# Performance work log

Hardware: AMD Instinct MI355X
Metric: run time of the kernel (lower is better)

Reference implementation:

```python
import jax, jax.numpy as jnp
import numpy as np

B, S, E, A, DK, H = 8, 2048, 256, 16, 64, 64  # batch, seq, embed, action, d_key, mlp hidden


def setup_inputs() -> dict:
    key = jax.random.key(0)
    ks = jax.random.split(key, 8)
    obs = jax.random.normal(ks[0], (B, S, E), dtype=jnp.float32)
    act = jnp.zeros((B, S, A), dtype=jnp.float32)  # one-hot actions; unused by forward
    # projection weights stored as [in, out] (torch Linear applies x @ W.T)
    Wq = jax.random.normal(ks[1], (E, DK), dtype=jnp.float32) / np.sqrt(E)
    Wk = jax.random.normal(ks[2], (E, DK), dtype=jnp.float32) / np.sqrt(E)
    Wv = jax.random.normal(ks[3], (E, DK), dtype=jnp.float32) / np.sqrt(E)
    W1 = jax.random.normal(ks[4], (DK, H), dtype=jnp.float32) / np.sqrt(DK)
    b1 = jnp.zeros((H,), dtype=jnp.float32)
    W2 = jax.random.normal(ks[5], (H, 1), dtype=jnp.float32) / np.sqrt(H)
    b2 = jnp.zeros((1,), dtype=jnp.float32)
    return dict(obs=obs, act=act, Wq=Wq, Wk=Wk, Wv=Wv, W1=W1, b1=b1, W2=W2, b2=b2)


def reference(obs, act, Wq, Wk, Wv, W1, b1, W2, b2):
    b, s, _ = obs.shape
    dk = Wq.shape[1]
    scale = dk ** -0.25  # applied to both q and k, net 1/sqrt(dk)
    q = (obs @ Wq) * scale          # [b, s, dk]
    k = (obs @ Wk) * scale          # [b, s, dk]
    v = obs @ Wv                    # [b, s, dk]
    scores = jnp.einsum('bqd,bkd->bqk', q, k)  # [b, s, s]
    causal = jnp.tril(jnp.ones((s, s), dtype=bool))
    scores = jnp.where(causal[None], scores, -jnp.inf)
    attn = jax.nn.softmax(scores, axis=2)      # [b, s, s]
    attn_out = jnp.einsum('bqk,bkd->bqd', attn, v)  # [b, s, dk]
    h = jax.nn.relu(attn_out.reshape(b * s, dk) @ W1 + b1)
    x = h @ W2 + b2                 # [b*s, 1]
    return (x, attn)
```

## Files before the change

### kernel.cpp

```cpp
#include <hip/hip_runtime.h>
#include <hip/hip_bf16.h>
#include <math.h>

#define NB 8
#define SQ 2048
#define NSP 8

typedef __attribute__((ext_vector_type(8))) short short8;
typedef __attribute__((ext_vector_type(4))) float f32x4;

__device__ __forceinline__ short f2bf(float f) {
    union { float f; unsigned u; } v; v.f = f;
    unsigned r = v.u + 0x7FFF + ((v.u >> 16) & 1);
    return (short)(r >> 16);
}

__global__ __launch_bounds__(256) void k_wt(const float* __restrict__ Wq,
                                            const float* __restrict__ Wk,
                                            const float* __restrict__ Wv,
                                            short* __restrict__ wt) {
    int o = blockIdx.x * 256 + threadIdx.x;
    int row = o >> 8, e = o & 255;
    int w = row >> 6, d = row & 63;
    const float* W = (w == 0) ? Wq : ((w == 1) ? Wk : Wv);
    wt[o] = f2bf(W[e * 64 + d]);
}

__global__ __launch_bounds__(256, 4) void k_proj(const float* __restrict__ obs,
                                                 const short* __restrict__ wt,
                                                 short* __restrict__ qw,
                                                 short* __restrict__ kw,
                                                 short* __restrict__ vt) {
    int tid = threadIdx.x, w = tid >> 6, l = tid & 63, lg = l >> 4, lc = l & 15;
    int r0 = blockIdx.x * 16;
    int arow = r0 + lc;
    f32x4 accq = {0.f,0.f,0.f,0.f}, acck = {0.f,0.f,0.f,0.f}, accv = {0.f,0.f,0.f,0.f};
    const short* wq = wt + (size_t)(w * 16 + lc) * 256;
    const short* wk = wt + (size_t)(64 + w * 16 + lc) * 256;
    const short* wv = wt + (size_t)(128 + w * 16 + lc) * 256;
    #pragma unroll
    for (int ks = 0; ks < 8; ++ks) {
        int e0 = ks * 32 + lg * 8;
        const float* ap = obs + (size_t)arow * 256 + e0;
        float4 f0 = *(const float4*)ap;
        float4 f1 = *(const float4*)(ap + 4);
        short8 a;
        a[0] = f2bf(f0.x); a[1] = f2bf(f0.y); a[2] = f2bf(f0.z); a[3] = f2bf(f0.w);
        a[4] = f2bf(f1.x); a[5] = f2bf(f1.y); a[6] = f2bf(f1.z); a[7] = f2bf(f1.w);
        accq = __builtin_amdgcn_mfma_f32_16x16x32_bf16(a, *(const short8*)(wq + e0), accq, 0, 0, 0);
        acck = __builtin_amdgcn_mfma_f32_16x16x32_bf16(a, *(const short8*)(wk + e0), acck, 0, 0, 0);
        accv = __builtin_amdgcn_mfma_f32_16x16x32_bf16(a, *(const short8*)(wv + e0), accv, 0, 0, 0);
    }
    const float scale = 0.35355339059327373f;
    __shared__ short ldsv[64][18];
    #pragma unroll
    for (int r = 0; r < 4; ++r) {
        int row = r0 + lg * 4 + r;
        qw[(size_t)row * 64 + w * 16 + lc] = f2bf(accq[r] * scale);
        kw[(size_t)row * 64 + w * 16 + lc] = f2bf(acck[r] * scale);
        ldsv[w * 16 + lc][lg * 4 + r] = f2bf(accv[r]);
    }
    __syncthreads();
    int b = r0 >> 11, s0 = r0 & 2047;
    int d = tid >> 2, sc = (tid & 3) * 4;
    short* dst = vt + (size_t)b * 64 * SQ + (size_t)d * SQ + s0 + sc;
    dst[0] = ldsv[d][sc]; dst[1] = ldsv[d][sc + 1];
    dst[2] = ldsv[d][sc + 2]; dst[3] = ldsv[d][sc + 3];
}

__global__ __launch_bounds__(256) void k_flash(const short* __restrict__ qw,
                                               const short* __restrict__ kw,
                                               const short* __restrict__ vt,
                                               float* __restrict__ op,
                                               float* __restrict__ lpart) {
    int qb = blockIdx.x, sp = blockIdx.y, b = blockIdx.z;
    if (sp > qb) return;
    int q0 = qb * 64;
    int tid = threadIdx.x, w = tid >> 6, l = tid & 63, lg = l >> 4, lc = l & 15;
    int r0 = q0 + w * 16;
    int eo = lg * 8;
    __shared__ short ldsP[4][16][72];
    const short* qbase = qw + (size_t)b * SQ * 64;
    const short* kbase = kw + (size_t)b * SQ * 64;
    const short* vbase = vt + (size_t)b * 64 * SQ;
    short8 qf0 = *(const short8*)(qbase + (size_t)(r0 + lc) * 64 + eo);
    short8 qf1 = *(const short8*)(qbase + (size_t)(r0 + lc) * 64 + 32 + eo);
    float lsum[4];
    f32x4 o[4];
    #pragma unroll
    for (int r = 0; r < 4; ++r) lsum[r] = 0.f;
    #pragma unroll
    for (int nj = 0; nj < 4; ++nj) o[nj] = (f32x4){0.f, 0.f, 0.f, 0.f};

    for (int kb = sp; kb <= qb; kb += NSP) {
        int k0 = kb * 64;
        f32x4 s[4];
        #pragma unroll
        for (int nj = 0; nj < 4; ++nj) s[nj] = (f32x4){0.f, 0.f, 0.f, 0.f};
        #pragma unroll
        for (int nj = 0; nj < 4; ++nj) {
            short8 kf = *(const short8*)(kbase + (size_t)(k0 + nj * 16 + lc) * 64 + eo);
            s[nj] = __builtin_amdgcn_mfma_f32_16x16x32_bf16(qf0, kf, s[nj], 0, 0, 0);
        }
        #pragma unroll
        for (int nj = 0; nj < 4; ++nj) {
            short8 kf = *(const short8*)(kbase + (size_t)(k0 + nj * 16 + lc) * 64 + 32 + eo);
            s[nj] = __builtin_amdgcn_mfma_f32_16x16x32_bf16(qf1, kf, s[nj], 0, 0, 0);
        }
        if (kb == qb) {
            #pragma unroll
            for (int nj = 0; nj < 4; ++nj)
                #pragma unroll
                for (int r = 0; r < 4; ++r)
                    if (k0 + nj * 16 + lc > r0 + lg * 4 + r) s[nj][r] = -INFINITY;
        }
        #pragma unroll
        for (int r = 0; r < 4; ++r) {
            float ps = 0.f;
            #pragma unroll
            for (int nj = 0; nj < 4; ++nj) {
                float p = __expf(s[nj][r]);
                ps += p;
                ldsP[w][lg * 4 + r][nj * 16 + lc] = f2bf(p);
            }
            ps += __shfl_xor(ps, 1);
            ps += __shfl_xor(ps, 2);
            ps += __shfl_xor(ps, 4);
            ps += __shfl_xor(ps, 8);
            lsum[r] += ps;
        }
        #pragma unroll
        for (int ks = 0; ks < 2; ++ks) {
            short8 pa = *(const short8*)&ldsP[w][lc][ks * 32 + lg * 8];
            #pragma unroll
            for (int nj = 0; nj < 4; ++nj) {
                short8 vf = *(const short8*)(vbase + (size_t)(nj * 16 + lc) * SQ + k0 + ks * 32 + eo);
                o[nj] = __builtin_amdgcn_mfma_f32_16x16x32_bf16(pa, vf, o[nj], 0, 0, 0);
            }
        }
    }
    size_t pb = ((size_t)sp * NB + b) * SQ;
    #pragma unroll
    for (int r = 0; r < 4; ++r) {
        int row = r0 + lg * 4 + r;
        if (lc == 0) lpart[pb + row] = lsum[r];
        #pragma unroll
        for (int nj = 0; nj < 4; ++nj)
            op[(pb + row) * 64 + nj * 16 + lc] = o[nj][r];
    }
}

__global__ __launch_bounds__(256) void k_combine(const float* __restrict__ op,
                                                 const float* __restrict__ lpart,
                                                 const float* __restrict__ W1,
                                                 const float* __restrict__ b1,
                                                 const float* __restrict__ W2,
                                                 const float* __restrict__ b2,
                                                 float* __restrict__ x,
                                                 float* __restrict__ linv) {
    int row0 = blockIdx.x * 8;
    int tid = threadIdx.x, w = tid >> 6, l = tid & 63;
    __shared__ float w1l[64][64];
    __shared__ float aol[8][64];
    {
        const float4* src = (const float4*)W1;
        float4* dst = (float4*)&w1l[0][0];
        #pragma unroll
        for (int i = 0; i < 4; ++i) dst[tid + i * 256] = src[tid + i * 256];
    }
    float inv2[2];
    #pragma unroll
    for (int rr = 0; rr < 2; ++rr) {
        int grow = row0 + w * 2 + rr;
        int b = grow >> 11, s = grow & 2047;
        int nsp = (s >> 6) + 1; if (nsp > NSP) nsp = NSP;
        float od = 0.f, lt = 0.f;
        for (int sp = 0; sp < nsp; ++sp) {
            size_t base = (size_t)(sp * NB + b) * SQ + s;
            od += op[base * 64 + l];
            lt += lpart[base];
        }
        float inv = 1.f / lt;
        inv2[rr] = inv;
        aol[w * 2 + rr][l] = od * inv;
        if (l == 0) linv[grow] = inv;
    }
    __syncthreads();
    #pragma unroll
    for (int rr = 0; rr < 2; ++rr) {
        int grow = row0 + w * 2 + rr;
        float t = b1[l];
        #pragma unroll 16
        for (int d = 0; d < 64; ++d) t += aol[w * 2 + rr][d] * w1l[d][l];
        float h = fmaxf(t, 0.f);
        float px = h * W2[l];
        px += __shfl_xor(px, 1);
        px += __shfl_xor(px, 2);
        px += __shfl_xor(px, 4);
        px += __shfl_xor(px, 8);
        px += __shfl_xor(px, 16);
        px += __shfl_xor(px, 32);
        if (l == 0) x[grow] = px + b2[0];
    }
    (void)inv2;
}

__global__ __launch_bounds__(256) void k_attnw(const short* __restrict__ qw,
                                               const short* __restrict__ kw,
                                               const float* __restrict__ linv,
                                               float* __restrict__ attn) {
    int kb = blockIdx.x, qb = blockIdx.y, b = blockIdx.z;
    int q0 = qb * 64, k0 = kb * 64;
    float* abase = attn + (size_t)b * SQ * SQ;
    int tid = threadIdx.x;
    if (kb > qb) {
        int row = q0 + (tid >> 2);
        float4* dst = (float4*)(abase + (size_t)row * SQ + k0 + (tid & 3) * 16);
        float4 z = {0.f, 0.f, 0.f, 0.f};
        dst[0] = z; dst[1] = z; dst[2] = z; dst[3] = z;
        return;
    }
    int w = tid >> 6, l = tid & 63, lg = l >> 4, lc = l & 15;
    int r0 = q0 + w * 16, eo = lg * 8;
    const short* qbase = qw + (size_t)b * SQ * 64;
    const short* kbase = kw + (size_t)b * SQ * 64;
    short8 qf0 = *(const short8*)(qbase + (size_t)(r0 + lc) * 64 + eo);
    short8 qf1 = *(const short8*)(qbase + (size_t)(r0 + lc) * 64 + 32 + eo);
    f32x4 s[4];
    #pragma unroll
    for (int nj = 0; nj < 4; ++nj) s[nj] = (f32x4){0.f, 0.f, 0.f, 0.f};
    #pragma unroll
    for (int nj = 0; nj < 4; ++nj) {
        short8 kf = *(const short8*)(kbase + (size_t)(k0 + nj * 16 + lc) * 64 + eo);
        s[nj] = __builtin_amdgcn_mfma_f32_16x16x32_bf16(qf0, kf, s[nj], 0, 0, 0);
    }
    #pragma unroll
    for (int nj = 0; nj < 4; ++nj) {
        short8 kf = *(const short8*)(kbase + (size_t)(k0 + nj * 16 + lc) * 64 + 32 + eo);
        s[nj] = __builtin_amdgcn_mfma_f32_16x16x32_bf16(qf1, kf, s[nj], 0, 0, 0);
    }
    #pragma unroll
    for (int r = 0; r < 4; ++r) {
        int row = r0 + lg * 4 + r;
        float iv = linv[(size_t)b * SQ + row];
        #pragma unroll
        for (int nj = 0; nj < 4; ++nj) {
            int col = k0 + nj * 16 + lc;
            float p = (col <= row) ? __expf(s[nj][r]) * iv : 0.f;
            abase[(size_t)row * SQ + col] = p;
        }
    }
}

extern "C" void kernel_launch(void* const* d_in, const int* in_sizes, int n_in,
                              void* d_out, int out_size, void* d_ws, size_t ws_size,
                              hipStream_t stream) {
    const float* obs = (const float*)d_in[0];
    const float* Wq  = (const float*)d_in[2];
    const float* Wk  = (const float*)d_in[3];
    const float* Wv  = (const float*)d_in[4];
    const float* W1  = (const float*)d_in[5];
    const float* b1  = (const float*)d_in[6];
    const float* W2  = (const float*)d_in[7];
    const float* b2  = (const float*)d_in[8];

    float* x    = (float*)d_out;
    float* attn = (float*)d_out + NB * SQ;

    float* op = attn;

    char* ws = (char*)d_ws;
    short* wt    = (short*)(ws);
    short* qw    = (short*)(ws + 131072);
    short* kw    = (short*)(ws + 2228224);
    short* vt    = (short*)(ws + 4325376);
    float* lpart = (float*)(ws + 6422528);
    float* linv  = (float*)(ws + 6946816);

    k_wt<<<dim3(192), dim3(256), 0, stream>>>(Wq, Wk, Wv, wt);
    k_proj<<<dim3(1024), dim3(256), 0, stream>>>(obs, wt, qw, kw, vt);
    k_flash<<<dim3(32, NSP, NB), dim3(256), 0, stream>>>(qw, kw, vt, op, lpart);
    k_combine<<<dim3(2048), dim3(256), 0, stream>>>(op, lpart, W1, b1, W2, b2, x, linv);
    k_attnw<<<dim3(32, 32, NB), dim3(256), 0, stream>>>(qw, kw, linv, attn);
}
```

Measured before the change: 158.8 us.

## Write unnormalized probabilities from flash kernel and rescale attention in separate pass

The flash kernel now stores exp(scores) straight into the attention output while it accumulates. A separate scaling kernel then multiplies by the inverse row sums and zeroes the upper triangle, replacing the kernel that recomputed QK^T. Row-sum reduction moves to its own small kernel, the partial-output buffer moves into workspace, and the number of key splits is halved. This removes the second QK^T recomputation but adds a read-modify-write pass over the lower-triangular attention matrix.

Result: faster. 140.4 us (-11.6%).

```diff
diff --git a/kernel.cpp b/kernel.cpp
--- a/kernel.cpp
+++ b/kernel.cpp
@@ -4,7 +4,7 @@
 
 #define NB 8
 #define SQ 2048
-#define NSP 8
+#define NSP 4
 
 typedef __attribute__((ext_vector_type(8))) short short8;
 typedef __attribute__((ext_vector_type(4))) float f32x4;
@@ -72,7 +72,8 @@
                                                const short* __restrict__ kw,
                                                const short* __restrict__ vt,
                                                float* __restrict__ op,
-                                               float* __restrict__ lpart) {
+                                               float* __restrict__ lpart,
+                                               float* __restrict__ attn) {
     int qb = blockIdx.x, sp = blockIdx.y, b = blockIdx.z;
     if (sp > qb) return;
     int q0 = qb * 64;
@@ -83,6 +84,7 @@
     const short* qbase = qw + (size_t)b * SQ * 64;
     const short* kbase = kw + (size_t)b * SQ * 64;
     const short* vbase = vt + (size_t)b * 64 * SQ;
+    float* abase = attn + (size_t)b * SQ * SQ;
     short8 qf0 = *(const short8*)(qbase + (size_t)(r0 + lc) * 64 + eo);
     short8 qf1 = *(const short8*)(qbase + (size_t)(r0 + lc) * 64 + 32 + eo);
     float lsum[4];
@@ -116,12 +118,14 @@
         }
         #pragma unroll
         for (int r = 0; r < 4; ++r) {
+            int row = r0 + lg * 4 + r;
             float ps = 0.f;
             #pragma unroll
             for (int nj = 0; nj < 4; ++nj) {
                 float p = __expf(s[nj][r]);
                 ps += p;
                 ldsP[w][lg * 4 + r][nj * 16 + lc] = f2bf(p);
+                abase[(size_t)row * SQ + k0 + nj * 16 + lc] = p;
             }
             ps += __shfl_xor(ps, 1);
             ps += __shfl_xor(ps, 2);
@@ -150,14 +154,23 @@
     }
 }
 
+__global__ __launch_bounds__(256) void k_lred(const float* __restrict__ lpart,
+                                              float* __restrict__ linv) {
+    int g = blockIdx.x * 256 + threadIdx.x;
+    int s = g & 2047, b = g >> 11;
+    int nsp = (s >> 6) + 1; if (nsp > NSP) nsp = NSP;
+    float t = 0.f;
+    for (int sp = 0; sp < nsp; ++sp) t += lpart[((size_t)sp * NB + b) * SQ + s];
+    linv[g] = 1.f / t;
+}
+
 __global__ __launch_bounds__(256) void k_combine(const float* __restrict__ op,
-                                                 const float* __restrict__ lpart,
+                                                 const float* __restrict__ linv,
                                                  const float* __restrict__ W1,
                                                  const float* __restrict__ b1,
                                                  const float* __restrict__ W2,
                                                  const float* __restrict__ b2,
-                                                 float* __restrict__ x,
-                                                 float* __restrict__ linv) {
+                                                 float* __restrict__ x) {
     int row0 = blockIdx.x * 8;
     int tid = threadIdx.x, w = tid >> 6, l = tid & 63;
     __shared__ float w1l[64][64];
@@ -168,22 +181,15 @@
         #pragma unroll
         for (int i = 0; i < 4; ++i) dst[tid + i * 256] = src[tid + i * 256];
     }
-    float inv2[2];
     #pragma unroll
     for (int rr = 0; rr < 2; ++rr) {
         int grow = row0 + w * 2 + rr;
         int b = grow >> 11, s = grow & 2047;
         int nsp = (s >> 6) + 1; if (nsp > NSP) nsp = NSP;
-        float od = 0.f, lt = 0.f;
-        for (int sp = 0; sp < nsp; ++sp) {
-            size_t base = (size_t)(sp * NB + b) * SQ + s;
-            od += op[base * 64 + l];
-            lt += lpart[base];
-        }
-        float inv = 1.f / lt;
-        inv2[rr] = inv;
-        aol[w * 2 + rr][l] = od * inv;
-        if (l == 0) linv[grow] = inv;
+        float od = 0.f;
+        for (int sp = 0; sp < nsp; ++sp)
+            od += op[(((size_t)sp * NB + b) * SQ + s) * 64 + l];
+        aol[w * 2 + rr][l] = od * linv[grow];
     }
     __syncthreads();
     #pragma unroll
@@ -202,53 +208,36 @@
         px += __shfl_xor(px, 32);
         if (l == 0) x[grow] = px + b2[0];
     }
-    (void)inv2;
-}
-
-__global__ __launch_bounds__(256) void k_attnw(const short* __restrict__ qw,
-                                               const short* __restrict__ kw,
-                                               const float* __restrict__ linv,
+}
+
+__global__ __launch_bounds__(256) void k_scale(const float* __restrict__ linv,
                                                float* __restrict__ attn) {
-    int kb = blockIdx.x, qb = blockIdx.y, b = blockIdx.z;
-    int q0 = qb * 64, k0 = kb * 64;
+    int csp = blockIdx.x, qb = blockIdx.y, b = blockIdx.z;
+    int tid = threadIdx.x, w = tid >> 6, l = tid & 63;
     float* abase = attn + (size_t)b * SQ * SQ;
-    int tid = threadIdx.x;
-    if (kb > qb) {
-        int row = q0 + (tid >> 2);
-        float4* dst = (float4*)(abase + (size_t)row * SQ + k0 + (tid & 3) * 16);
+    int colb = csp * 256 + l * 4;
+    if (csp * 4 > qb) {
         float4 z = {0.f, 0.f, 0.f, 0.f};
-        dst[0] = z; dst[1] = z; dst[2] = z; dst[3] = z;
+        #pragma unroll
+        for (int r = 0; r < 16; ++r) {
+            int row = qb * 64 + w * 16 + r;
+            *(float4*)(abase + (size_t)row * SQ + colb) = z;
+        }
         return;
     }
-    int w = tid >> 6, l = tid & 63, lg = l >> 4, lc = l & 15;
-    int r0 = q0 + w * 16, eo = lg * 8;
-    const short* qbase = qw + (size_t)b * SQ * 64;
-    const short* kbase = kw + (size_t)b * SQ * 64;
-    short8 qf0 = *(const short8*)(qbase + (size_t)(r0 + lc) * 64 + eo);
-    short8 qf1 = *(const short8*)(qbase + (size_t)(r0 + lc) * 64 + 32 + eo);
-    f32x4 s[4];
-    #pragma unroll
-    for (int nj = 0; nj < 4; ++nj) s[nj] = (f32x4){0.f, 0.f, 0.f, 0.f};
-    #pragma unroll
-    for (int nj = 0; nj < 4; ++nj) {
-        short8 kf = *(const short8*)(kbase + (size_t)(k0 + nj * 16 + lc) * 64 + eo);
-        s[nj] = __builtin_amdgcn_mfma_f32_16x16x32_bf16(qf0, kf, s[nj], 0, 0, 0);
-    }
-    #pragma unroll
-    for (int nj = 0; nj < 4; ++nj) {
-        short8 kf = *(const short8*)(kbase + (size_t)(k0 + nj * 16 + lc) * 64 + 32 + eo);
-        s[nj] = __builtin_amdgcn_mfma_f32_16x16x32_bf16(qf1, kf, s[nj], 0, 0, 0);
-    }
-    #pragma unroll
-    for (int r = 0; r < 4; ++r) {
-        int row = r0 + lg * 4 + r;
-        float iv = linv[(size_t)b * SQ + row];
-        #pragma unroll
-        for (int nj = 0; nj < 4; ++nj) {
-            int col = k0 + nj * 16 + lc;
-            float p = (col <= row) ? __expf(s[nj][r]) * iv : 0.f;
-            abase[(size_t)row * SQ + col] = p;
-        }
+    #pragma unroll
+    for (int r = 0; r < 16; ++r) {
+        int row = qb * 64 + w * 16 + r;
+        float inv = linv[(size_t)b * SQ + row];
+        int lim = row | 63;
+        float* p = abase + (size_t)row * SQ + colb;
+        float4 v = *(const float4*)p;
+        float4 o;
+        o.x = (colb + 0 <= lim) ? v.x * inv : 0.f;
+        o.y = (colb + 1 <= lim) ? v.y * inv : 0.f;
+        o.z = (colb + 2 <= lim) ? v.z * inv : 0.f;
+        o.w = (colb + 3 <= lim) ? v.w * inv : 0.f;
+        *(float4*)p = o;
     }
 }
 
@@ -267,19 +256,19 @@
     float* x    = (float*)d_out;
     float* attn = (float*)d_out + NB * SQ;
 
-    float* op = attn;
-
     char* ws = (char*)d_ws;
     short* wt    = (short*)(ws);
     short* qw    = (short*)(ws + 131072);
     short* kw    = (short*)(ws + 2228224);
     short* vt    = (short*)(ws + 4325376);
     float* lpart = (float*)(ws + 6422528);
-    float* linv  = (float*)(ws + 6946816);
+    float* linv  = (float*)(ws + 6684672);
+    float* op    = (float*)(ws + 6750208);
 
     k_wt<<<dim3(192), dim3(256), 0, stream>>>(Wq, Wk, Wv, wt);
     k_proj<<<dim3(1024), dim3(256), 0, stream>>>(obs, wt, qw, kw, vt);
-    k_flash<<<dim3(32, NSP, NB), dim3(256), 0, stream>>>(qw, kw, vt, op, lpart);
-    k_combine<<<dim3(2048), dim3(256), 0, stream>>>(op, lpart, W1, b1, W2, b2, x, linv);
-    k_attnw<<<dim3(32, 32, NB), dim3(256), 0, stream>>>(qw, kw, linv, attn);
-}
+    k_flash<<<dim3(32, NSP, NB), dim3(256), 0, stream>>>(qw, kw, vt, op, lpart, attn);
+    k_lred<<<dim3(64), dim3(256), 0, stream>>>(lpart, linv);
+    k_combine<<<dim3(2048), dim3(256), 0, stream>>>(op, linv, W1, b1, W2, b2, x);
+    k_scale<<<dim3(8, 32, NB), dim3(256), 0, stream>>>(linv, attn);
+}
```
